# Optimization experiments

Measured on AMD Instinct MI355X. Metric: run time of the kernel, lower is better.

Reference implementation:

```python
import jax, jax.numpy as jnp
import numpy as np

PI = 3.14159  # constant used in the torch module
N_QUBITS = 10
N_LAYERS = 4
B = 1024  # number of graphs


def _lin_init(k, fan_in, fan_out):
    k1, k2 = jax.random.split(k)
    s = 1.0 / np.sqrt(fan_in)
    W = jax.random.uniform(k1, (fan_in, fan_out), jnp.float32, -s, s)
    b = jax.random.uniform(k2, (fan_out,), jnp.float32, -s, s)
    return W, b


def setup_inputs():
    key = jax.random.key(0)
    ks = jax.random.split(key, 12)
    N, E, Fin, H, Emb = 32768, 131072, 128, 256, 128
    x = jax.random.normal(ks[0], (N, Fin), jnp.float32)
    edge_index = jax.random.randint(ks[1], (2, E), 0, N)
    batch = jnp.sort(jax.random.randint(ks[2], (N,), 0, B))
    edge_attr = jax.random.uniform(ks[3], (E, 4), dtype=jnp.float32)
    W1, b1 = _lin_init(ks[4], Fin, H)          # GCNConv 1
    W2, b2 = _lin_init(ks[5], H, Emb)          # GCNConv 2
    projW, projb = _lin_init(ks[6], Emb, N_QUBITS)
    vqc_weights = jax.random.uniform(ks[7], (N_LAYERS, N_QUBITS), jnp.float32, 0.0, 2 * np.pi)
    epW, epb = _lin_init(ks[8], 4, N_QUBITS - 1)
    cW1, cb1 = _lin_init(ks[9], Emb + N_QUBITS, 16)
    cW2, cb2 = _lin_init(ks[10], 16, 1)
    return dict(x=x, edge_index=edge_index, batch=batch, edge_attr=edge_attr,
                W1=W1, b1=b1, W2=W2, b2=b2, projW=projW, projb=projb,
                vqc_weights=vqc_weights, epW=epW, epb=epb,
                cW1=cW1, cb1=cb1, cW2=cW2, cb2=cb2)


def _gcn_conv(x, W, b, src, dst, n):
    # GCNConv with self-loops: sym-normalized aggregation of xW
    h = x @ W
    deg = jnp.zeros((n,), x.dtype).at[dst].add(1.0) + 1.0  # +1 self-loop
    dinv = jax.lax.rsqrt(deg)
    coef = (dinv[src] * dinv[dst])[:, None]
    agg = jnp.zeros_like(h).at[dst].add(h[src] * coef)
    return agg + h * (1.0 / deg)[:, None] + b


def _segment_mean(v, seg, n):
    tot = jnp.zeros((n, v.shape[1]), v.dtype).at[seg].add(v)
    cnt = jnp.zeros((n,), v.dtype).at[seg].add(1.0)
    return tot / jnp.clip(cnt, 1.0)[:, None]


def _run_vqc(q_in, weights, ep):
    # Batched real state-vector simulation. All gates (RY, CRY) are real.
    # Wire 0 = most significant bit (pennylane default.qubit convention).
    b = q_in.shape[0]
    dim = 2 ** N_QUBITS
    st = jnp.zeros((b, dim), q_in.dtype).at[:, 0].set(1.0)

    def ry(st, theta, w):
        th = jnp.broadcast_to(theta, (b,)) * 0.5
        c = jnp.cos(th)[:, None, None]
        s = jnp.sin(th)[:, None, None]
        r = st.reshape(b, 2 ** w, 2, -1)
        a0, a1 = r[:, :, 0], r[:, :, 1]
        return jnp.stack([c * a0 - s * a1, s * a0 + c * a1], axis=2).reshape(b, dim)

    def cry(st, theta, w):
        # control w, target w+1 (adjacent wires)
        th = jnp.broadcast_to(theta, (b,)) * 0.5
        c = jnp.cos(th)[:, None, None]
        s = jnp.sin(th)[:, None, None]
        r = st.reshape(b, 2 ** w, 2, 2, -1)
        a0, a1 = r[:, :, 1, 0], r[:, :, 1, 1]
        r = r.at[:, :, 1, 0].set(c * a0 - s * a1).at[:, :, 1, 1].set(s * a0 + c * a1)
        return r.reshape(b, dim)

    for i in range(N_QUBITS):                      # AngleEmbedding (RY)
        st = ry(st, q_in[:, i], i)
    for layer in range(N_LAYERS):
        for i in range(N_QUBITS):
            st = ry(st, weights[layer, i], i)
        for i in range(N_QUBITS - 1):
            st = cry(st, ep[:, i], i)

    probs = st * st
    zs = []
    for i in range(N_QUBITS):
        p = probs.reshape(b, 2 ** i, 2, -1).sum(axis=(1, 3))
        zs.append(p[:, 0] - p[:, 1])               # <PauliZ(i)>
    return jnp.stack(zs, axis=1)                   # [B, n_qubits]


def reference(x, edge_index, batch, edge_attr, W1, b1, W2, b2, projW, projb,
              vqc_weights, epW, epb, cW1, cb1, cW2, cb2):
    N = x.shape[0]
    src, dst = edge_index[0], edge_index[1]
    # GCN encoder: two GCNConv + ReLU, global mean pool (dropout = eval mode)
    h = jax.nn.relu(_gcn_conv(x, W1, b1, src, dst, N))
    h = jax.nn.relu(_gcn_conv(h, W2, b2, src, dst, N))
    emb = _segment_mean(h, batch, B)               # [B, gcn_embed]

    q_in = jnp.tanh(emb @ projW + projb) * PI      # [B, n_qubits]

    # scatter-mean edge pooling per graph, then edge projection
    edge_batch = batch[src]
    pooled_edge = _segment_mean(edge_attr, edge_batch, B)  # [B, 4]
    ep = pooled_edge @ epW + epb                   # [B, n_qubits-1]

    q_out = _run_vqc(q_in, vqc_weights, ep)        # [B, n_qubits]

    combined = jnp.concatenate([emb, q_out], axis=-1)
    hid = jax.nn.relu(combined @ cW1 + cb1)
    return hid @ cW2 + cb2                         # [B, num_tasks]
```

## Files before the change

### kernel.cpp

```cpp
#include <hip/hip_runtime.h>

#define PI_F 3.14159f
#define NQ 10
#define PB 64

__global__ void k_zero(float4* __restrict__ p, int n4) {
  int i = blockIdx.x * blockDim.x + threadIdx.x;
  int stride = gridDim.x * blockDim.x;
  float4 z = {0.f, 0.f, 0.f, 0.f};
  for (; i < n4; i += stride) p[i] = z;
}

__global__ void k_count(const int* __restrict__ dstA, int E, int* __restrict__ cnt) {
  int e = blockIdx.x * blockDim.x + threadIdx.x;
  if (e < E) atomicAdd(&cnt[dstA[e]], 1);
}

__global__ __launch_bounds__(1024) void k_edge_pool(const int* __restrict__ srcA,
                                                    const int* __restrict__ batch,
                                                    const float* __restrict__ eattr, int E,
                                                    float* __restrict__ part) {
  __shared__ float bins[1024 * 5];
  int t = threadIdx.x;
  for (int i = t; i < 5120; i += 1024) bins[i] = 0.f;
  __syncthreads();
  int per = (E + gridDim.x - 1) / gridDim.x;
  int base = blockIdx.x * per;
  int end = min(base + per, E);
  for (int e = base + t; e < end; e += 1024) {
    int s = srcA[e];
    int g = batch[s];
    float4 v = *(const float4*)(eattr + (size_t)e * 4);
    atomicAdd(&bins[g * 5 + 0], v.x);
    atomicAdd(&bins[g * 5 + 1], v.y);
    atomicAdd(&bins[g * 5 + 2], v.z);
    atomicAdd(&bins[g * 5 + 3], v.w);
    atomicAdd(&bins[g * 5 + 4], 1.0f);
  }
  __syncthreads();
  float* dst = part + (size_t)blockIdx.x * 5120;
  for (int i = t; i < 5120; i += 1024) dst[i] = bins[i];
}

__global__ __launch_bounds__(1024) void k_scan1(const int* __restrict__ cnt,
                                                int* __restrict__ incl,
                                                int* __restrict__ bsum) {
  __shared__ int buf[1024];
  int t = threadIdx.x;
  int base = blockIdx.x << 10;
  buf[t] = cnt[base + t];
  __syncthreads();
#pragma unroll
  for (int off = 1; off < 1024; off <<= 1) {
    int x = (t >= off) ? buf[t - off] : 0;
    __syncthreads();
    buf[t] += x;
    __syncthreads();
  }
  incl[base + t] = buf[t];
  if (t == 1023) bsum[blockIdx.x] = buf[t];
}

__global__ void k_node_setup(const int* __restrict__ cnt, const int* __restrict__ incl,
                             const int* __restrict__ bsum, const int* __restrict__ batch,
                             int N, int Bn, int* __restrict__ rowStart,
                             int* __restrict__ pos, float* __restrict__ dinv,
                             float* __restrict__ invdeg, int* __restrict__ starts) {
  int i = blockIdx.x * blockDim.x + threadIdx.x;
  if (i >= N) return;
  int blk = i >> 10;
  int pre = 0;
  for (int j = 0; j < blk; j++) pre += bsum[j];
  int c = cnt[i];
  int inc = incl[i] + pre;
  rowStart[i + 1] = inc;
  pos[i] = inc - c;
  if (i == 0) rowStart[0] = 0;
  float d = (float)c + 1.0f;
  dinv[i] = 1.0f / sqrtf(d);
  invdeg[i] = 1.0f / d;
  int b = batch[i];
  int bp = (i == 0) ? -1 : batch[i - 1];
  for (int g = bp + 1; g <= b; g++) starts[g] = i;
  if (i == N - 1) {
    for (int g = b + 1; g <= Bn; g++) starts[g] = N;
  }
}

__global__ void k_fill(const int* __restrict__ dst, const int* __restrict__ srcA,
                       const float* __restrict__ dinv, int E, int* __restrict__ pos,
                       int* __restrict__ srcSorted, float* __restrict__ dcoef) {
  int e = blockIdx.x * blockDim.x + threadIdx.x;
  if (e >= E) return;
  int s = srcA[e];
  int slot = atomicAdd(&pos[dst[e]], 1);
  srcSorted[slot] = s;
  dcoef[slot] = dinv[s];
}

__global__ __launch_bounds__(256) void k_gemm(const float* __restrict__ A,
                                              const float* __restrict__ B,
                                              float* __restrict__ C,
                                              int M, int K, int N) {
  __shared__ float As[64][36];
  __shared__ float Bs[32][68];
  int t = threadIdx.x;
  int tx = t & 15, ty = t >> 4;
  int row0 = blockIdx.y * 64, col0 = blockIdx.x * 64;
  float acc[4][4] = {};
  for (int k0 = 0; k0 < K; k0 += 32) {
#pragma unroll
    for (int rep = 0; rep < 2; rep++) {
      int slot = t + rep * 256;
      int r = slot >> 3;
      int cg = (slot & 7) << 2;
      float4 v = *(const float4*)(A + (size_t)(row0 + r) * K + (k0 + cg));
      *(float4*)&As[r][cg] = v;
      int r2 = slot >> 4;
      int cg2 = (slot & 15) << 2;
      float4 w = *(const float4*)(B + (size_t)(k0 + r2) * N + (col0 + cg2));
      *(float4*)&Bs[r2][cg2] = w;
    }
    __syncthreads();
#pragma unroll
    for (int kk = 0; kk < 32; kk++) {
      float av[4];
      av[0] = As[ty * 4 + 0][kk];
      av[1] = As[ty * 4 + 1][kk];
      av[2] = As[ty * 4 + 2][kk];
      av[3] = As[ty * 4 + 3][kk];
      float4 b4 = *(const float4*)&Bs[kk][tx << 2];
      float bv[4] = {b4.x, b4.y, b4.z, b4.w};
#pragma unroll
      for (int i = 0; i < 4; i++)
#pragma unroll
        for (int j = 0; j < 4; j++) acc[i][j] = fmaf(av[i], bv[j], acc[i][j]);
    }
    __syncthreads();
  }
#pragma unroll
  for (int i = 0; i < 4; i++) {
    float4 v = {acc[i][0], acc[i][1], acc[i][2], acc[i][3]};
    *(float4*)(C + (size_t)(row0 + ty * 4 + i) * N + (col0 + (tx << 2))) = v;
  }
}

__global__ __launch_bounds__(256) void k_gcn_combine(
    const float* __restrict__ hlin, const int* __restrict__ srcSorted,
    const float* __restrict__ dcoef, const int* __restrict__ rowStart,
    const float* __restrict__ dinv, const float* __restrict__ invdeg,
    const float* __restrict__ bias, float* __restrict__ hout, int N, int C, int shift) {
  int gid = blockIdx.x * blockDim.x + threadIdx.x;
  int n = gid >> shift;
  if (n >= N) return;
  int cq = (gid & ((1 << shift) - 1)) << 2;
  int e0 = rowStart[n], e1 = rowStart[n + 1];
  float di = dinv[n];
  float ax = 0.f, ay = 0.f, az = 0.f, aw = 0.f;
  for (int e = e0; e < e1; e++) {
    int s = srcSorted[e];
    float coef = dcoef[e] * di;
    float4 v = *(const float4*)(hlin + (size_t)s * C + cq);
    ax = fmaf(coef, v.x, ax);
    ay = fmaf(coef, v.y, ay);
    az = fmaf(coef, v.z, az);
    aw = fmaf(coef, v.w, aw);
  }
  float idg = invdeg[n];
  float4 hv = *(const float4*)(hlin + (size_t)n * C + cq);
  float4 bv = *(const float4*)(bias + cq);
  float4 r;
  r.x = fmaxf(fmaf(hv.x, idg, ax) + bv.x, 0.f);
  r.y = fmaxf(fmaf(hv.y, idg, ay) + bv.y, 0.f);
  r.z = fmaxf(fmaf(hv.z, idg, az) + bv.z, 0.f);
  r.w = fmaxf(fmaf(hv.w, idg, aw) + bv.w, 0.f);
  *(float4*)(hout + (size_t)n * C + cq) = r;
}

__global__ __launch_bounds__(256) void k_segmean(const float* __restrict__ h2,
                                                 const int* __restrict__ starts,
                                                 float* __restrict__ emb) {
  __shared__ float tmp[128];
  int g = blockIdx.x;
  int t = threadIdx.x;
  int c = t & 127;
  int half = t >> 7;
  int s0 = starts[g], s1 = starts[g + 1];
  float inv = 1.0f / (float)(s1 - s0 > 0 ? s1 - s0 : 1);
  float sum = 0.f;
  for (int i = s0 + half; i < s1; i += 2) sum += h2[(size_t)i * 128 + c];
  if (half == 0) tmp[c] = sum;
  __syncthreads();
  if (half == 1) emb[(size_t)g * 128 + c] = (tmp[c] + sum) * inv;
}

__global__ __launch_bounds__(256) void k_angles(
    const float* __restrict__ emb, const float* __restrict__ part,
    const float* __restrict__ projW, const float* __restrict__ projb,
    const float* __restrict__ epW, const float* __restrict__ epb, int Bn,
    float* __restrict__ angc, float* __restrict__ angs) {
  int wid = (blockIdx.x * blockDim.x + threadIdx.x) >> 6;
  int lane = threadIdx.x & 63;
  int g = wid / 11;
  int a = wid - g * 11;
  if (g >= Bn) return;
  if (a < 10) {
    float2 v = *(const float2*)(emb + (size_t)g * 128 + lane * 2);
    float s = v.x * projW[(lane * 2) * NQ + a] + v.y * projW[(lane * 2 + 1) * NQ + a];
#pragma unroll
    for (int off = 32; off >= 1; off >>= 1) s += __shfl_down(s, off, 64);
    if (lane == 0) {
      float th = tanhf(s + projb[a]) * PI_F * 0.5f;
      angc[g * 19 + a] = cosf(th);
      angs[g * 19 + a] = sinf(th);
    }
  } else {
    const float* pp = part + (size_t)lane * 5120 + g * 5;
    float p0 = pp[0], p1 = pp[1], p2 = pp[2], p3 = pp[3], p4 = pp[4];
#pragma unroll
    for (int off = 32; off >= 1; off >>= 1) {
      p0 += __shfl_down(p0, off, 64);
      p1 += __shfl_down(p1, off, 64);
      p2 += __shfl_down(p2, off, 64);
      p3 += __shfl_down(p3, off, 64);
      p4 += __shfl_down(p4, off, 64);
    }
    p0 = __shfl(p0, 0, 64);
    p1 = __shfl(p1, 0, 64);
    p2 = __shfl(p2, 0, 64);
    p3 = __shfl(p3, 0, 64);
    p4 = __shfl(p4, 0, 64);
    if (lane < 9) {
      float icnt = 1.0f / fmaxf(p4, 1.0f);
      float sum = epb[lane];
      sum = fmaf(p0 * icnt, epW[0 * 9 + lane], sum);
      sum = fmaf(p1 * icnt, epW[1 * 9 + lane], sum);
      sum = fmaf(p2 * icnt, epW[2 * 9 + lane], sum);
      sum = fmaf(p3 * icnt, epW[3 * 9 + lane], sum);
      float th = sum * 0.5f;
      angc[g * 19 + 10 + lane] = cosf(th);
      angs[g * 19 + 10 + lane] = sinf(th);
    }
  }
}

template <int B>
__device__ __forceinline__ void ry_reg(float* st, float c, float s) {
#pragma unroll
  for (int j = 0; j < 16; j++) {
    if (!(j & (1 << B))) {
      float x0 = st[j], x1 = st[j | (1 << B)];
      st[j] = c * x0 - s * x1;
      st[j | (1 << B)] = fmaf(s, x0, c * x1);
    }
  }
}

template <int LB>
__device__ __forceinline__ void ry_lane(float* st, float c, float s, int lane) {
  bool hi = (lane >> LB) & 1;
#pragma unroll
  for (int j = 0; j < 16; j++) {
    float p = __shfl_xor(st[j], 1 << LB, 64);
    float a = c * st[j] - s * p;
    float b = fmaf(s, p, c * st[j]);
    st[j] = hi ? b : a;
  }
}

template <int LC, int LT>
__device__ __forceinline__ void cry_ll(float* st, float c, float s, int lane) {
  bool ctrl = (lane >> LC) & 1;
  bool hi = (lane >> LT) & 1;
#pragma unroll
  for (int j = 0; j < 16; j++) {
    float p = __shfl_xor(st[j], 1 << LT, 64);
    float a = c * st[j] - s * p;
    float b = fmaf(s, p, c * st[j]);
    float nv = hi ? b : a;
    st[j] = ctrl ? nv : st[j];
  }
}

__device__ __forceinline__ void cry_l0r3(float* st, float c, float s, int lane) {
  bool ctrl = lane & 1;
#pragma unroll
  for (int j = 0; j < 8; j++) {
    float x0 = st[j], x1 = st[j + 8];
    float n0 = c * x0 - s * x1;
    float n1 = fmaf(s, x0, c * x1);
    st[j] = ctrl ? n0 : x0;
    st[j + 8] = ctrl ? n1 : x1;
  }
}

template <int BC, int BT>
__device__ __forceinline__ void cry_rr(float* st, float c, float s) {
#pragma unroll
  for (int j = 0; j < 16; j++) {
    if ((j & (1 << BC)) && !(j & (1 << BT))) {
      float x0 = st[j], x1 = st[j | (1 << BT)];
      st[j] = c * x0 - s * x1;
      st[j | (1 << BT)] = fmaf(s, x0, c * x1);
    }
  }
}

#define RY_LAYER(base)                                    \
  ry_lane<5>(st, csc[(base) + 0], css[(base) + 0], lane); \
  ry_lane<4>(st, csc[(base) + 1], css[(base) + 1], lane); \
  ry_lane<3>(st, csc[(base) + 2], css[(base) + 2], lane); \
  ry_lane<2>(st, csc[(base) + 3], css[(base) + 3], lane); \
  ry_lane<1>(st, csc[(base) + 4], css[(base) + 4], lane); \
  ry_lane<0>(st, csc[(base) + 5], css[(base) + 5], lane); \
  ry_reg<3>(st, csc[(base) + 6], css[(base) + 6]);        \
  ry_reg<2>(st, csc[(base) + 7], css[(base) + 7]);        \
  ry_reg<1>(st, csc[(base) + 8], css[(base) + 8]);        \
  ry_reg<0>(st, csc[(base) + 9], css[(base) + 9]);

#define CRY_LAYER()                            \
  cry_ll<5, 4>(st, csc[50], css[50], lane);    \
  cry_ll<4, 3>(st, csc[51], css[51], lane);    \
  cry_ll<3, 2>(st, csc[52], css[52], lane);    \
  cry_ll<2, 1>(st, csc[53], css[53], lane);    \
  cry_ll<1, 0>(st, csc[54], css[54], lane);    \
  cry_l0r3(st, csc[55], css[55], lane);        \
  cry_rr<3, 2>(st, csc[56], css[56]);          \
  cry_rr<2, 1>(st, csc[57], css[57]);          \
  cry_rr<1, 0>(st, csc[58], css[58]);

__global__ __launch_bounds__(64) void k_vqc_head(
    const float* __restrict__ emb, const float* __restrict__ angc,
    const float* __restrict__ angs, const float* __restrict__ vqcW,
    const float* __restrict__ cW1, const float* __restrict__ cb1,
    const float* __restrict__ cW2, const float* __restrict__ cb2,
    float* __restrict__ out) {
  int g = blockIdx.x;
  int lane = threadIdx.x;
  __shared__ float semb[128];
  __shared__ float csc[59], css[59];
  __shared__ float zq[NQ];

  {
    float2 v = *(const float2*)(emb + (size_t)g * 128 + lane * 2);
    semb[lane * 2] = v.x;
    semb[lane * 2 + 1] = v.y;
  }
  if (lane < NQ) {
    csc[lane] = angc[g * 19 + lane];
    css[lane] = angs[g * 19 + lane];
  } else if (lane < 50) {
    float th = vqcW[lane - NQ] * 0.5f;
    csc[lane] = cosf(th);
    css[lane] = sinf(th);
  } else if (lane < 59) {
    csc[lane] = angc[g * 19 + 10 + (lane - 50)];
    css[lane] = angs[g * 19 + 10 + (lane - 50)];
  }
  __syncthreads();

  float st[16];
#pragma unroll
  for (int j = 0; j < 16; j++) st[j] = 0.f;
  if (lane == 0) st[0] = 1.f;

  RY_LAYER(0);
  RY_LAYER(10); CRY_LAYER();
  RY_LAYER(20); CRY_LAYER();
  RY_LAYER(30); CRY_LAYER();
  RY_LAYER(40); CRY_LAYER();

  float p[16];
  float tot = 0.f;
#pragma unroll
  for (int j = 0; j < 16; j++) {
    p[j] = st[j] * st[j];
    tot += p[j];
  }
  float z[NQ];
#pragma unroll
  for (int i = 0; i < 6; i++) {
    int LB = 5 - i;
    z[i] = ((lane >> LB) & 1) ? -tot : tot;
  }
#pragma unroll
  for (int i = 6; i < 10; i++) {
    int B = 9 - i;
    float a = 0.f;
#pragma unroll
    for (int j = 0; j < 16; j++) a += ((j >> B) & 1) ? -p[j] : p[j];
    z[i] = a;
  }
#pragma unroll
  for (int off = 32; off >= 1; off >>= 1)
#pragma unroll
    for (int i = 0; i < 10; i++) z[i] += __shfl_down(z[i], off, 64);
  if (lane == 0) {
#pragma unroll
    for (int i = 0; i < 10; i++) zq[i] = z[i];
  }
  __syncthreads();

  int o = lane & 15, cch = lane >> 4;
  float sum = 0.f;
#pragma unroll
  for (int t = 0; t < 32; t++) {
    int k = cch * 32 + t;
    sum = fmaf(semb[k], cW1[k * 16 + o], sum);
  }
  if (cch == 3) {
#pragma unroll
    for (int k = 0; k < 10; k++) sum = fmaf(zq[k], cW1[(128 + k) * 16 + o], sum);
  }
  sum += __shfl_down(sum, 32, 64);
  sum += __shfl_down(sum, 16, 64);
  float hv = fmaxf(sum + cb1[o], 0.f);
  float ov = (lane < 16) ? hv * cW2[lane] : 0.f;
  ov += __shfl_down(ov, 8, 64);
  ov += __shfl_down(ov, 4, 64);
  ov += __shfl_down(ov, 2, 64);
  ov += __shfl_down(ov, 1, 64);
  if (lane == 0) out[g] = ov + cb2[0];
}

extern "C" void kernel_launch(void* const* d_in, const int* in_sizes, int n_in,
                              void* d_out, int out_size, void* d_ws, size_t ws_size,
                              hipStream_t stream) {
  const float* x = (const float*)d_in[0];
  const int* ei = (const int*)d_in[1];
  const int* batch = (const int*)d_in[2];
  const float* eattr = (const float*)d_in[3];
  const float* W1 = (const float*)d_in[4];
  const float* b1 = (const float*)d_in[5];
  const float* W2 = (const float*)d_in[6];
  const float* b2 = (const float*)d_in[7];
  const float* projW = (const float*)d_in[8];
  const float* projb = (const float*)d_in[9];
  const float* vqcW = (const float*)d_in[10];
  const float* epW = (const float*)d_in[11];
  const float* epb = (const float*)d_in[12];
  const float* cW1 = (const float*)d_in[13];
  const float* cb1 = (const float*)d_in[14];
  const float* cW2 = (const float*)d_in[15];
  const float* cb2 = (const float*)d_in[16];
  float* out = (float*)d_out;

  const int N = in_sizes[0] / 128;
  const int E = in_sizes[1] / 2;
  const int Bn = out_size;

  const int* srcA = ei;
  const int* dstA = ei + E;

  char* ws = (char*)d_ws;
  float* bufA = (float*)ws;
  float* bufB = (float*)(ws + ((size_t)32 << 20));
  size_t off = (size_t)64 << 20;
  auto alloc = [&](size_t bytes) {
    size_t o = off;
    off += (bytes + 255) & ~(size_t)255;
    return o;
  };
  int* cnt = (int*)(ws + alloc((size_t)N * 4));
  size_t zeroEnd = off;
  float* part = (float*)(ws + alloc((size_t)PB * 5120 * 4));
  int* rowStart = (int*)(ws + alloc((size_t)(N + 1) * 4));
  int* pos = (int*)(ws + alloc((size_t)N * 4));
  int* srcSorted = (int*)(ws + alloc((size_t)E * 4));
  float* dcoef = (float*)(ws + alloc((size_t)E * 4));
  float* dinv = (float*)(ws + alloc((size_t)N * 4));
  float* invdeg = (float*)(ws + alloc((size_t)N * 4));
  int* starts = (int*)(ws + alloc((size_t)(Bn + 1) * 4));
  int* incl = (int*)(ws + alloc((size_t)N * 4));
  int* bsum = (int*)(ws + alloc(64 * 4));
  float* emb = (float*)(ws + alloc((size_t)Bn * 128 * 4));
  float* angc = (float*)(ws + alloc((size_t)Bn * 19 * 4));
  float* angs = (float*)(ws + alloc((size_t)Bn * 19 * 4));

  int eblocks = (E + 255) / 256;
  int nblocks = (N + 255) / 256;
  int nb1024 = N >> 10;

  int zero4 = (int)((zeroEnd - ((size_t)64 << 20)) / 16);
  k_zero<<<(zero4 + 255) / 256, 256, 0, stream>>>((float4*)(ws + ((size_t)64 << 20)), zero4);

  k_count<<<eblocks, 256, 0, stream>>>(dstA, E, cnt);
  k_edge_pool<<<PB, 1024, 0, stream>>>(srcA, batch, eattr, E, part);
  k_scan1<<<nb1024, 1024, 0, stream>>>(cnt, incl, bsum);
  k_node_setup<<<nblocks, 256, 0, stream>>>(cnt, incl, bsum, batch, N, Bn, rowStart, pos,
                                            dinv, invdeg, starts);
  k_fill<<<eblocks, 256, 0, stream>>>(dstA, srcA, dinv, E, pos, srcSorted, dcoef);

  {
    dim3 grid(256 / 64, N / 64);
    k_gemm<<<grid, 256, 0, stream>>>(x, W1, bufA, N, 128, 256);
  }
  k_gcn_combine<<<(N * 64) / 256, 256, 0, stream>>>(bufA, srcSorted, dcoef, rowStart,
                                                    dinv, invdeg, b1, bufB, N, 256, 6);
  {
    dim3 grid(128 / 64, N / 64);
    k_gemm<<<grid, 256, 0, stream>>>(bufB, W2, bufA, N, 256, 128);
  }
  k_gcn_combine<<<(N * 32) / 256, 256, 0, stream>>>(bufA, srcSorted, dcoef, rowStart,
                                                    dinv, invdeg, b2, bufB, N, 128, 5);
  k_segmean<<<Bn, 256, 0, stream>>>(bufB, starts, emb);
  {
    int waves = Bn * 11;
    k_angles<<<(waves + 3) / 4, 256, 0, stream>>>(emb, part, projW, projb, epW, epb, Bn,
                                                  angc, angs);
  }
  k_vqc_head<<<Bn, 64, 0, stream>>>(emb, angc, angs, vqcW, cW1, cb1, cW2, cb2, out);
}
```

Before: 199.7 us.

## Enlarge GEMM tiles to 128x128 with 8x8 register blocking and transposed A tile

```diff
diff --git a/kernel.cpp b/kernel.cpp
--- a/kernel.cpp
+++ b/kernel.cpp
@@ -102,46 +102,51 @@
                                               const float* __restrict__ B,
                                               float* __restrict__ C,
                                               int M, int K, int N) {
-  __shared__ float As[64][36];
-  __shared__ float Bs[32][68];
+  __shared__ float As[32][132];
+  __shared__ float Bs[32][132];
   int t = threadIdx.x;
   int tx = t & 15, ty = t >> 4;
-  int row0 = blockIdx.y * 64, col0 = blockIdx.x * 64;
-  float acc[4][4] = {};
+  int row0 = blockIdx.y * 128, col0 = blockIdx.x * 128;
+  float acc[8][8] = {};
   for (int k0 = 0; k0 < K; k0 += 32) {
-#pragma unroll
-    for (int rep = 0; rep < 2; rep++) {
+    __syncthreads();
+#pragma unroll
+    for (int rep = 0; rep < 4; rep++) {
       int slot = t + rep * 256;
       int r = slot >> 3;
       int cg = (slot & 7) << 2;
       float4 v = *(const float4*)(A + (size_t)(row0 + r) * K + (k0 + cg));
-      *(float4*)&As[r][cg] = v;
-      int r2 = slot >> 4;
-      int cg2 = (slot & 15) << 2;
-      float4 w = *(const float4*)(B + (size_t)(k0 + r2) * N + (col0 + cg2));
-      *(float4*)&Bs[r2][cg2] = w;
+      As[cg + 0][r] = v.x;
+      As[cg + 1][r] = v.y;
+      As[cg + 2][r] = v.z;
+      As[cg + 3][r] = v.w;
+      int r2 = slot >> 5;
+      int c2 = (slot & 31) << 2;
+      float4 w = *(const float4*)(B + (size_t)(k0 + r2) * N + (col0 + c2));
+      *(float4*)&Bs[r2][c2] = w;
     }
     __syncthreads();
-#pragma unroll
+#pragma unroll 4
     for (int kk = 0; kk < 32; kk++) {
-      float av[4];
-      av[0] = As[ty * 4 + 0][kk];
-      av[1] = As[ty * 4 + 1][kk];
-      av[2] = As[ty * 4 + 2][kk];
-      av[3] = As[ty * 4 + 3][kk];
-      float4 b4 = *(const float4*)&Bs[kk][tx << 2];
-      float bv[4] = {b4.x, b4.y, b4.z, b4.w};
-#pragma unroll
-      for (int i = 0; i < 4; i++)
-#pragma unroll
-        for (int j = 0; j < 4; j++) acc[i][j] = fmaf(av[i], bv[j], acc[i][j]);
-    }
-    __syncthreads();
-  }
-#pragma unroll
-  for (int i = 0; i < 4; i++) {
-    float4 v = {acc[i][0], acc[i][1], acc[i][2], acc[i][3]};
-    *(float4*)(C + (size_t)(row0 + ty * 4 + i) * N + (col0 + (tx << 2))) = v;
+      float4 a0 = *(const float4*)&As[kk][ty << 3];
+      float4 a1 = *(const float4*)&As[kk][(ty << 3) + 4];
+      float4 b0 = *(const float4*)&Bs[kk][tx << 3];
+      float4 b1 = *(const float4*)&Bs[kk][(tx << 3) + 4];
+      float av[8] = {a0.x, a0.y, a0.z, a0.w, a1.x, a1.y, a1.z, a1.w};
+      float bv[8] = {b0.x, b0.y, b0.z, b0.w, b1.x, b1.y, b1.z, b1.w};
+#pragma unroll
+      for (int i = 0; i < 8; i++)
+#pragma unroll
+        for (int j = 0; j < 8; j++) acc[i][j] = fmaf(av[i], bv[j], acc[i][j]);
+    }
+  }
+#pragma unroll
+  for (int i = 0; i < 8; i++) {
+    float* cp = C + (size_t)(row0 + (ty << 3) + i) * N + col0 + (tx << 3);
+    float4 v0 = {acc[i][0], acc[i][1], acc[i][2], acc[i][3]};
+    float4 v1 = {acc[i][4], acc[i][5], acc[i][6], acc[i][7]};
+    *(float4*)cp = v0;
+    *(float4*)(cp + 4) = v1;
   }
 }
 
@@ -306,29 +311,6 @@
   }
 }
 
-#define RY_LAYER(base)                                    \
-  ry_lane<5>(st, csc[(base) + 0], css[(base) + 0], lane); \
-  ry_lane<4>(st, csc[(base) + 1], css[(base) + 1], lane); \
-  ry_lane<3>(st, csc[(base) + 2], css[(base) + 2], lane); \
-  ry_lane<2>(st, csc[(base) + 3], css[(base) + 3], lane); \
-  ry_lane<1>(st, csc[(base) + 4], css[(base) + 4], lane); \
-  ry_lane<0>(st, csc[(base) + 5], css[(base) + 5], lane); \
-  ry_reg<3>(st, csc[(base) + 6], css[(base) + 6]);        \
-  ry_reg<2>(st, csc[(base) + 7], css[(base) + 7]);        \
-  ry_reg<1>(st, csc[(base) + 8], css[(base) + 8]);        \
-  ry_reg<0>(st, csc[(base) + 9], css[(base) + 9]);
-
-#define CRY_LAYER()                            \
-  cry_ll<5, 4>(st, csc[50], css[50], lane);    \
-  cry_ll<4, 3>(st, csc[51], css[51], lane);    \
-  cry_ll<3, 2>(st, csc[52], css[52], lane);    \
-  cry_ll<2, 1>(st, csc[53], css[53], lane);    \
-  cry_ll<1, 0>(st, csc[54], css[54], lane);    \
-  cry_l0r3(st, csc[55], css[55], lane);        \
-  cry_rr<3, 2>(st, csc[56], css[56]);          \
-  cry_rr<2, 1>(st, csc[57], css[57]);          \
-  cry_rr<1, 0>(st, csc[58], css[58]);
-
 __global__ __launch_bounds__(64) void k_vqc_head(
     const float* __restrict__ emb, const float* __restrict__ angc,
     const float* __restrict__ angs, const float* __restrict__ vqcW,
@@ -364,11 +346,31 @@
   for (int j = 0; j < 16; j++) st[j] = 0.f;
   if (lane == 0) st[0] = 1.f;
 
-  RY_LAYER(0);
-  RY_LAYER(10); CRY_LAYER();
-  RY_LAYER(20); CRY_LAYER();
-  RY_LAYER(30); CRY_LAYER();
-  RY_LAYER(40); CRY_LAYER();
+#pragma unroll 1
+  for (int L = 0; L < 5; L++) {
+    int b = L * 10;
+    ry_lane<5>(st, csc[b + 0], css[b + 0], lane);
+    ry_lane<4>(st, csc[b + 1], css[b + 1], lane);
+    ry_lane<3>(st, csc[b + 2], css[b + 2], lane);
+    ry_lane<2>(st, csc[b + 3], css[b + 3], lane);
+    ry_lane<1>(st, csc[b + 4], css[b + 4], lane);
+    ry_lane<0>(st, csc[b + 5], css[b + 5], lane);
+    ry_reg<3>(st, csc[b + 6], css[b + 6]);
+    ry_reg<2>(st, csc[b + 7], css[b + 7]);
+    ry_reg<1>(st, csc[b + 8], css[b + 8]);
+    ry_reg<0>(st, csc[b + 9], css[b + 9]);
+    if (b) {
+      cry_ll<5, 4>(st, csc[50], css[50], lane);
+      cry_ll<4, 3>(st, csc[51], css[51], lane);
+      cry_ll<3, 2>(st, csc[52], css[52], lane);
+      cry_ll<2, 1>(st, csc[53], css[53], lane);
+      cry_ll<1, 0>(st, csc[54], css[54], lane);
+      cry_l0r3(st, csc[55], css[55], lane);
+      cry_rr<3, 2>(st, csc[56], css[56]);
+      cry_rr<2, 1>(st, csc[57], css[57]);
+      cry_rr<1, 0>(st, csc[58], css[58]);
+    }
+  }
 
   float p[16];
   float tot = 0.f;
@@ -492,13 +494,13 @@
   k_fill<<<eblocks, 256, 0, stream>>>(dstA, srcA, dinv, E, pos, srcSorted, dcoef);
 
   {
-    dim3 grid(256 / 64, N / 64);
+    dim3 grid(256 / 128, N / 128);
     k_gemm<<<grid, 256, 0, stream>>>(x, W1, bufA, N, 128, 256);
   }
   k_gcn_combine<<<(N * 64) / 256, 256, 0, stream>>>(bufA, srcSorted, dcoef, rowStart,
                                                     dinv, invdeg, b1, bufB, N, 256, 6);
   {
-    dim3 grid(128 / 64, N / 64);
+    dim3 grid(128 / 128, N / 128);
     k_gemm<<<grid, 256, 0, stream>>>(bufB, W2, bufA, N, 256, 128);
   }
   k_gcn_combine<<<(N * 32) / 256, 256, 0, stream>>>(bufA, srcSorted, dcoef, rowStart,
```

New measurement: 219.2 us. 1.1x slower.
